# Optimization experiments

Measured on AMD Instinct MI355X. Metric: run time of the kernel, lower is better.

The kernel has to match this reference:

```python
import jax, jax.numpy as jnp
import numpy as np

B, T, N, D = 8, 24, 263, 512
N0, N1 = 32, 64
SEG = 12
LAMBDA_INIT = 0.8 - 0.6 * float(np.exp(-0.3 * (1 - 1)))  # layer_idx=1 -> 0.2


def _ln(x, g, b, eps=1e-5):
    m = jnp.mean(x, axis=-1, keepdims=True)
    v = jnp.var(x, axis=-1, keepdims=True)
    return (x - m) * jax.lax.rsqrt(v + eps) * g + b


def _proj(x, W):
    # 1x1 Conv2d over channel dim == per-position linear, W: [out, in]
    return jnp.einsum('btnd,ed->btne', x, W)


def _forward(x, agg_x0, agg_x1, tmp_map,
             Wq_s, Wk_s, Wv_s, lq1, lk1, lq2, lk2, ln_g, ln_b,
             Wq_a0, Wk_a0, Wv_a0, Wq_a1, Wk_a1, Wv_a1, M0, M1, Wagg, bagg,
             Wq_t, Wk_t, Wv_t, q_agg, Wk_tg, Wv_tg, Wout, bout):
    B, T, N, D = x.shape
    # ---- SpatialDiffAttn: spa_dim=256, heads=4, head_dim=32 (2*32 per head) ----
    H, dh = 4, 32
    q = _proj(x, Wq_s).reshape(B, T, N, H, 2 * dh)
    k = _proj(x, Wk_s).reshape(B, T, N, H, 2 * dh)
    v = _proj(x, Wv_s).reshape(B, T, N, H, 2 * dh)
    q1, q2 = q[..., :dh], q[..., dh:]
    k1, k2 = k[..., :dh], k[..., dh:]
    sc = dh ** -0.5
    # attn11/attn12 share softmax(q1 k1^T); cat([p1@v1, p1@v2]) == p1 @ v_full
    p1 = jax.nn.softmax(jnp.einsum('btnhd,btmhd->bthnm', q1, k1) * sc, axis=-1)
    a1 = jnp.einsum('bthnm,btmhe->btnhe', p1, v)
    p2 = jax.nn.softmax(jnp.einsum('btnhd,btmhd->bthnm', q2, k2) * sc, axis=-1)
    a2 = jnp.einsum('bthnm,btmhe->btnhe', p2, v)
    lam = jnp.exp(jnp.sum(lq1 * lk1)) - jnp.exp(jnp.sum(lq2 * lk2)) + LAMBDA_INIT
    s_x = (_ln(a1 - lam * a2, ln_g, ln_b) * (1.0 - LAMBDA_INIT)).reshape(B, T, N, H * 2 * dh)

    # ---- SpatialAttn aggregated branches (agg_dim=128, heads=2, head_dim=64) ----
    def agg_branch(ax, Wq, Wk, Wv, M):
        Ni = ax.shape[2]
        Ha, dha = 2, 64
        qa = _proj(ax, Wq).reshape(B, T, Ni, Ha, dha)
        ka = _proj(ax, Wk).reshape(B, T, Ni, Ha, dha)
        va = _proj(ax, Wv).reshape(B, T, Ni, Ha, dha)
        pa = jax.nn.softmax(jnp.einsum('btnhd,btmhd->bthnm', qa, ka) * (dha ** -0.5), axis=-1)
        sx = jnp.einsum('bthnm,btmhd->bthnd', pa, va)          # [B,T,Ha,Ni,dha]
        # cls_map = M^T -> pool Ni clusters up to N regions
        return jnp.einsum('mn,bthmd->btnhd', M, sx).reshape(B, T, N, Ha * dha)

    sg = agg_branch(agg_x0, Wq_a0, Wk_a0, Wv_a0, M0) + agg_branch(agg_x1, Wq_a1, Wk_a1, Wv_a1, M1)
    sg = sg @ Wagg.T + bagg

    # ---- TemporalAttn (tmp_dim=128, heads=2, head_dim=64) ----
    Ht, dht = 2, 64
    qt = _proj(x, Wq_t).reshape(B, T, N, Ht, dht)
    kt = _proj(x, Wk_t).reshape(B, T, N, Ht, dht)
    vt = _proj(x, Wv_t).reshape(B, T, N, Ht, dht)
    pt = jax.nn.softmax(jnp.einsum('btnhd,bsnhd->bnhts', qt, kt) * (dht ** -0.5), axis=-1)
    t_x = jnp.einsum('bnhts,bsnhd->btnhd', pt, vt).reshape(B, T, N, Ht * dht)

    # ---- TemporalAttn aggregated (learned query, seg_num=12) ----
    S = q_agg.shape[1]
    qg = q_agg.reshape(N, S, Ht, dht)
    kg = _proj(x, Wk_tg).reshape(B, T, N, Ht, dht)
    vg = _proj(x, Wv_tg).reshape(B, T, N, Ht, dht)
    pg = jax.nn.softmax(jnp.einsum('nshd,btnhd->bnhst', qg, kg) * (dht ** -0.5), axis=-1)
    tgx = jnp.einsum('bnhst,btnhd->bnshd', pg, vg).reshape(B, N, S, Ht * dht)
    tg = jnp.einsum('bnts,bnsd->btnd', tmp_map, tgx)           # [B,T,N,128]

    st = jnp.concatenate([s_x, sg, t_x, tg], axis=-1)          # [B,T,N,640]
    return st @ Wout.T + bout


def setup_inputs() -> dict:
    ks = jax.random.split(jax.random.key(0), 32)
    r = lambda i, shape, s=0.05: (jax.random.normal(ks[i], shape) * s).astype(jnp.float32)
    return dict(
        x=r(0, (B, T, N, D), 1.0),
        agg_x0=r(1, (B, T, N0, D), 1.0),
        agg_x1=r(2, (B, T, N1, D), 1.0),
        tmp_map=jax.random.uniform(ks[3], (B, N, T, SEG), dtype=jnp.float32),
        Wq_s=r(4, (256, D)), Wk_s=r(5, (256, D)), Wv_s=r(6, (256, D)),
        lq1=r(7, (32,), 0.1), lk1=r(8, (32,), 0.1), lq2=r(9, (32,), 0.1), lk2=r(10, (32,), 0.1),
        ln_g=jnp.ones((64,), jnp.float32), ln_b=jnp.zeros((64,), jnp.float32),
        Wq_a0=r(11, (128, D)), Wk_a0=r(12, (128, D)), Wv_a0=r(13, (128, D)),
        Wq_a1=r(14, (128, D)), Wk_a1=r(15, (128, D)), Wv_a1=r(16, (128, D)),
        M0=r(17, (N0, N), 0.1), M1=r(18, (N1, N), 0.1),
        Wagg=r(19, (128, 128)), bagg=jnp.zeros((128,), jnp.float32),
        Wq_t=r(20, (128, D)), Wk_t=r(21, (128, D)), Wv_t=r(22, (128, D)),
        q_agg=r(23, (N, SEG, 128), 1.0),
        Wk_tg=r(24, (128, D)), Wv_tg=r(25, (128, D)),
        Wout=r(26, (D, 640)), bout=jnp.zeros((D,), jnp.float32),
    )


def reference(x, agg_x0, agg_x1, tmp_map,
              Wq_s, Wk_s, Wv_s, lq1, lk1, lq2, lk2, ln_g, ln_b,
              Wq_a0, Wk_a0, Wv_a0, Wq_a1, Wk_a1, Wv_a1, M0, M1, Wagg, bagg,
              Wq_t, Wk_t, Wv_t, q_agg, Wk_tg, Wv_tg, Wout, bout):
    return _forward(x, agg_x0, agg_x1, tmp_map,
                    Wq_s, Wk_s, Wv_s, lq1, lk1, lq2, lk2, ln_g, ln_b,
                    Wq_a0, Wk_a0, Wv_a0, Wq_a1, Wk_a1, Wv_a1, M0, M1, Wagg, bagg,
                    Wq_t, Wk_t, Wv_t, q_agg, Wk_tg, Wv_tg, Wout, bout)
```

## Files before the change

### kernel.cpp

```cpp
#include <hip/hip_runtime.h>

#define NN 263
#define TT 24

typedef __fp16 h2 __attribute__((ext_vector_type(2)));
typedef _Float16 f16x4 __attribute__((ext_vector_type(4)));
typedef _Float16 f16x8 __attribute__((ext_vector_type(8)));
typedef float f32x4 __attribute__((ext_vector_type(4)));

struct WSegs  { const float* p[6]; };
struct WSegsH { const _Float16* p[6]; };
struct CvtSegs { const float* src[11]; _Float16* dst[11]; int cnt8[11]; };

static __device__ __forceinline__ float wred_sum(float v) {
  #pragma unroll
  for (int off = 32; off >= 1; off >>= 1) v += __shfl_xor(v, off, 64);
  return v;
}
static __device__ __forceinline__ float wred_max(float v) {
  #pragma unroll
  for (int off = 32; off >= 1; off >>= 1) v = fmaxf(v, __shfl_xor(v, off, 64));
  return v;
}

__global__ __launch_bounds__(256) void cvt_f16(CvtSegs cs, int nseg, int total8)
{
  const int stride = gridDim.x * 256;
  for (int i = blockIdx.x * 256 + threadIdx.x; i < total8; i += stride) {
    int r = i, s = 0;
    while (s < nseg - 1 && r >= cs.cnt8[s]) { r -= cs.cnt8[s]; ++s; }
    const float* sp = cs.src[s] + (size_t)r * 8;
    float4 a = *(const float4*)sp;
    float4 b = *(const float4*)(sp + 4);
    union { h2 h[4]; f16x8 v; } u;
    u.h[0] = __builtin_amdgcn_cvt_pkrtz(a.x, a.y);
    u.h[1] = __builtin_amdgcn_cvt_pkrtz(a.z, a.w);
    u.h[2] = __builtin_amdgcn_cvt_pkrtz(b.x, b.y);
    u.h[3] = __builtin_amdgcn_cvt_pkrtz(b.z, b.w);
    *(f16x8*)(cs.dst[s] + (size_t)r * 8) = u.v;
  }
}

template<int OUT_HALF>
__global__ __launch_bounds__(256) void gemm_h16(
    const _Float16* __restrict__ A, WSegsH wsg, const float* __restrict__ bias,
    void* __restrict__ Cp, int M, int NT, int K, int ldc)
{
  __shared__ _Float16 As[2][128][40];
  __shared__ _Float16 Bs[2][128][40];
  const int tid  = threadIdx.x;
  const int lane = tid & 63;
  const int wave = tid >> 6;
  const int wr = wave >> 1, wc = wave & 1;

  const int nwg = gridDim.x;
  const int q8 = nwg >> 3, r8 = nwg & 7;
  const int xcd = blockIdx.x & 7, pos = blockIdx.x >> 3;
  const int logical = (xcd < r8 ? xcd * (q8 + 1) : r8 * (q8 + 1) + (xcd - r8) * q8) + pos;
  const int bm = (logical / NT) * 128;
  const int bn = logical - (logical / NT) * NT;
  const _Float16* __restrict__ W = wsg.p[bn];

  const int srow = tid >> 2;
  const int sch  = (tid & 3) * 8;
  const _Float16* aptr[2];
  const _Float16* bptr[2];
  #pragma unroll
  for (int l = 0; l < 2; ++l) {
    int gm = bm + srow + 64 * l; if (gm > M - 1) gm = M - 1;
    aptr[l] = A + (size_t)gm * K + sch;
    bptr[l] = W + (size_t)(srow + 64 * l) * K + sch;
  }

  f32x4 acc[4][4];
  #pragma unroll
  for (int i = 0; i < 4; ++i)
    #pragma unroll
    for (int j = 0; j < 4; ++j) {
      acc[i][j].x = 0.f; acc[i][j].y = 0.f; acc[i][j].z = 0.f; acc[i][j].w = 0.f;
    }

  const int fr = lane & 15;
  const int fk = (lane >> 4) * 8;

  f16x8 av[2], bv[2];
  av[0] = *(const f16x8*)aptr[0]; av[1] = *(const f16x8*)aptr[1];
  bv[0] = *(const f16x8*)bptr[0]; bv[1] = *(const f16x8*)bptr[1];

  int cur = 0;
  for (int k0 = 0; k0 < K; k0 += 32, cur ^= 1) {
    *(f16x8*)&As[cur][srow     ][sch] = av[0];
    *(f16x8*)&As[cur][srow + 64][sch] = av[1];
    *(f16x8*)&Bs[cur][srow     ][sch] = bv[0];
    *(f16x8*)&Bs[cur][srow + 64][sch] = bv[1];
    if (k0 + 32 < K) {
      av[0] = *(const f16x8*)(aptr[0] + k0 + 32);
      av[1] = *(const f16x8*)(aptr[1] + k0 + 32);
      bv[0] = *(const f16x8*)(bptr[0] + k0 + 32);
      bv[1] = *(const f16x8*)(bptr[1] + k0 + 32);
    }
    __syncthreads();

    f16x8 af[4], bf[4];
    #pragma unroll
    for (int mi = 0; mi < 4; ++mi)
      af[mi] = *(const f16x8*)&As[cur][wr * 64 + mi * 16 + fr][fk];
    #pragma unroll
    for (int ni = 0; ni < 4; ++ni)
      bf[ni] = *(const f16x8*)&Bs[cur][wc * 64 + ni * 16 + fr][fk];
    #pragma unroll
    for (int mi = 0; mi < 4; ++mi)
      #pragma unroll
      for (int ni = 0; ni < 4; ++ni)
        acc[mi][ni] = __builtin_amdgcn_mfma_f32_16x16x32_f16(
            af[mi], bf[ni], acc[mi][ni], 0, 0, 0);
  }

  #pragma unroll
  for (int mi = 0; mi < 4; ++mi) {
    int rb = bm + wr * 64 + mi * 16 + (lane >> 4) * 4;
    #pragma unroll
    for (int r = 0; r < 4; ++r) {
      int gm = rb + r;
      if (gm < M) {
        int gn = bn * 128 + wc * 64 + fr;
        #pragma unroll
        for (int ni = 0; ni < 4; ++ni) {
          float v = acc[mi][ni][r];
          if (bias) v += bias[gn + ni * 16];
          if (OUT_HALF) {
            ((_Float16*)Cp)[(size_t)gm * ldc + gn + ni * 16] = (_Float16)v;
          } else {
            ((float*)Cp)[(size_t)gm * ldc + gn + ni * 16] = v;
          }
        }
      }
    }
  }
}

__global__ __launch_bounds__(256) void gemm_nt_mfma(
    const float* __restrict__ A, WSegs ws, const float* __restrict__ bias,
    float* __restrict__ C, int M, int NT, int K, int ldc)
{
  __shared__ _Float16 As[128][40];
  __shared__ _Float16 Bs[128][40];
  const int tid  = threadIdx.x;
  const int lane = tid & 63;
  const int wave = tid >> 6;
  const int wr = wave >> 1, wc = wave & 1;

  const int nwg = gridDim.x;
  const int q8 = nwg >> 3, r8 = nwg & 7;
  const int xcd = blockIdx.x & 7, pos = blockIdx.x >> 3;
  const int logical = (xcd < r8 ? xcd * (q8 + 1) : r8 * (q8 + 1) + (xcd - r8) * q8) + pos;
  const int bm = (logical / NT) * 128;
  const int bn = logical - (logical / NT) * NT;
  const float* __restrict__ W = ws.p[bn];

  const int srow = tid >> 3;
  const int skq  = (tid & 7) * 4;
  const float* aptr[4];
  const float* bptr[4];
  #pragma unroll
  for (int l = 0; l < 4; ++l) {
    int gm = bm + srow + 32 * l; if (gm > M - 1) gm = M - 1;
    aptr[l] = A + (size_t)gm * K + skq;
    bptr[l] = W + (size_t)(srow + 32 * l) * K + skq;
  }

  f32x4 acc[4][4];
  #pragma unroll
  for (int i = 0; i < 4; ++i)
    #pragma unroll
    for (int j = 0; j < 4; ++j) {
      acc[i][j].x = 0.f; acc[i][j].y = 0.f; acc[i][j].z = 0.f; acc[i][j].w = 0.f;
    }

  const int fr = lane & 15;
  const int fk = (lane >> 4) * 8;

  float4 av[4], bv[4];
  #pragma unroll
  for (int l = 0; l < 4; ++l) {
    av[l] = *(const float4*)(aptr[l]);
    bv[l] = *(const float4*)(bptr[l]);
  }

  for (int k0 = 0; k0 < K; k0 += 32) {
    #pragma unroll
    for (int l = 0; l < 4; ++l) {
      f16x4 a4, b4;
      a4.x = (_Float16)av[l].x; a4.y = (_Float16)av[l].y;
      a4.z = (_Float16)av[l].z; a4.w = (_Float16)av[l].w;
      b4.x = (_Float16)bv[l].x; b4.y = (_Float16)bv[l].y;
      b4.z = (_Float16)bv[l].z; b4.w = (_Float16)bv[l].w;
      *(f16x4*)&As[srow + 32 * l][skq] = a4;
      *(f16x4*)&Bs[srow + 32 * l][skq] = b4;
    }
    __syncthreads();

    if (k0 + 32 < K) {
      #pragma unroll
      for (int l = 0; l < 4; ++l) {
        av[l] = *(const float4*)(aptr[l] + k0 + 32);
        bv[l] = *(const float4*)(bptr[l] + k0 + 32);
      }
    }

    f16x8 af[4], bf[4];
    #pragma unroll
    for (int mi = 0; mi < 4; ++mi)
      af[mi] = *(const f16x8*)&As[wr * 64 + mi * 16 + fr][fk];
    #pragma unroll
    for (int ni = 0; ni < 4; ++ni)
      bf[ni] = *(const f16x8*)&Bs[wc * 64 + ni * 16 + fr][fk];
    #pragma unroll
    for (int mi = 0; mi < 4; ++mi)
      #pragma unroll
      for (int ni = 0; ni < 4; ++ni)
        acc[mi][ni] = __builtin_amdgcn_mfma_f32_16x16x32_f16(
            af[mi], bf[ni], acc[mi][ni], 0, 0, 0);
    __syncthreads();
  }

  #pragma unroll
  for (int mi = 0; mi < 4; ++mi) {
    int rb = bm + wr * 64 + mi * 16 + (lane >> 4) * 4;
    #pragma unroll
    for (int r = 0; r < 4; ++r) {
      int gm = rb + r;
      if (gm < M) {
        int gn = bn * 128 + wc * 64 + fr;
        float* crow = C + (size_t)gm * ldc + gn;
        #pragma unroll
        for (int ni = 0; ni < 4; ++ni) {
          float v = acc[mi][ni][r];
          if (bias) v += bias[gn + ni * 16];
          crow[ni * 16] = v;
        }
      }
    }
  }
}

__global__ void lam_kernel(const float* __restrict__ lq1, const float* __restrict__ lk1,
                           const float* __restrict__ lq2, const float* __restrict__ lk2,
                           float* __restrict__ out) {
  int lane = threadIdx.x;
  float v1 = lane < 32 ? lq1[lane] * lk1[lane] : 0.f;
  float v2 = lane < 32 ? lq2[lane] * lk2[lane] : 0.f;
  v1 = wred_sum(v1);
  v2 = wred_sum(v2);
  if (lane == 0) out[0] = expf(v1) - expf(v2) + 0.2f;
}

__global__ __launch_bounds__(512, 2) void diff_attn(
    const _Float16* __restrict__ qkv, _Float16* __restrict__ aout)
{
  __shared__ _Float16 Ks[2][272][40];
  __shared__ h2 Vt[64][148];
  __shared__ h2 Pb[8][16][148];

  const int h  = blockIdx.x & 3;
  const int bt = blockIdx.x >> 2;
  const int tid = threadIdx.x;
  const int lane = tid & 63;
  const int wave = tid >> 6;
  const int fr = lane & 15;
  const int kb = (lane >> 4) * 4;
  const _Float16* base = qkv + (size_t)bt * NN * 768;

  for (int idx = tid; idx < 272 * 8; idx += 512) {
    int row = idx >> 3, c = idx & 7;
    int sr = row < NN ? row : NN - 1;
    f16x8 kv = *(const f16x8*)(base + (size_t)sr * 768 + 256 + h * 64 + c * 8);
    *(f16x8*)&Ks[c >> 2][row][(c & 3) * 8] = kv;
  }
  {
    const ushort* vb = (const ushort*)(base + 512 + h * 64);
    for (int idx = tid; idx < 64 * 37; idx += 512) {
      int d = idx & 63, kp0 = (idx >> 6) * 4;
      union { ushort u[8]; f16x8 v; } w;
      #pragma unroll
      for (int i = 0; i < 4; ++i) {
        int kp = kp0 + i;
        ushort lo = 0, hi = 0;
        if (kp < 136) {
          int m0 = 2 * kp, m1 = 2 * kp + 1;
          if (m0 > NN - 1) m0 = NN - 1;
          if (m1 > NN - 1) m1 = NN - 1;
          lo = vb[(size_t)m0 * 768 + d];
          hi = vb[(size_t)m1 * 768 + d];
        }
        w.u[2 * i] = lo; w.u[2 * i + 1] = hi;
      }
      *(f16x8*)&Vt[d][kp0] = w.v;
    }
  }
  {
    h2 z; z.x = (__fp16)0.f; z.y = (__fp16)0.f;
    #pragma unroll
    for (int t = 0; t < 3; ++t) Pb[wave][fr][136 + (kb >> 2) * 3 + t] = z;
  }
  __syncthreads();

  const float scq = 0.17677669529663687f;

  for (int task = wave; task < 34; task += 8) {
    const int chunk = task >> 1;
    const int half  = task & 1;

    int qsrc = chunk * 16 + fr; if (qsrc > NN - 1) qsrc = NN - 1;
    f16x8 qf = *(const f16x8*)(base + (size_t)qsrc * 768 + h * 64 + half * 32 + kb * 2);

    f32x4 s[17];
    #pragma unroll
    for (int mt = 0; mt < 17; ++mt) {
      f16x8 af = *(const f16x8*)&Ks[half][mt * 16 + fr][kb * 2];
      f32x4 z4 = {0.f, 0.f, 0.f, 0.f};
      s[mt] = __builtin_amdgcn_mfma_f32_16x16x32_f16(af, qf, z4, 0, 0, 0);
    }

    float mx4[4] = {-1e30f, -1e30f, -1e30f, -1e30f};
    #pragma unroll
    for (int mt = 0; mt < 17; ++mt)
      #pragma unroll
      for (int r = 0; r < 4; ++r) {
        float v = s[mt][r] * scq;
        if (mt * 16 + kb + r >= NN) v = -1e30f;
        s[mt][r] = v;
        mx4[r] = fmaxf(mx4[r], v);
      }
    float mx = fmaxf(fmaxf(mx4[0], mx4[1]), fmaxf(mx4[2], mx4[3]));
    mx = fmaxf(mx, __shfl_xor(mx, 16, 64));
    mx = fmaxf(mx, __shfl_xor(mx, 32, 64));
    float sm4[4] = {0.f, 0.f, 0.f, 0.f};
    #pragma unroll
    for (int mt = 0; mt < 17; ++mt)
      #pragma unroll
      for (int r = 0; r < 4; ++r) {
        float p = __expf(s[mt][r] - mx);
        s[mt][r] = p;
        sm4[r] += p;
      }
    float sum = (sm4[0] + sm4[1]) + (sm4[2] + sm4[3]);
    sum += __shfl_xor(sum, 16, 64);
    sum += __shfl_xor(sum, 32, 64);
    float inv = 1.f / sum;

    #pragma unroll
    for (int mt = 0; mt < 17; ++mt) {
      union { h2 h[2]; f16x4 v; } pw;
      pw.h[0] = __builtin_amdgcn_cvt_pkrtz(s[mt][0] * inv, s[mt][1] * inv);
      pw.h[1] = __builtin_amdgcn_cvt_pkrtz(s[mt][2] * inv, s[mt][3] * inv);
      *(f16x4*)&Pb[wave][fr][8 * mt + (kb >> 1)] = pw.v;
    }

    f32x4 o[4];
    #pragma unroll
    for (int nt = 0; nt < 4; ++nt) {
      o[nt].x = 0.f; o[nt].y = 0.f; o[nt].z = 0.f; o[nt].w = 0.f;
    }
    #pragma unroll
    for (int s9 = 0; s9 < 9; ++s9) {
      f16x8 pa = *(const f16x8*)&Pb[wave][fr][16 * s9 + kb];
      #pragma unroll
      for (int nt = 0; nt < 4; ++nt) {
        f16x8 vb2 = *(const f16x8*)&Vt[nt * 16 + fr][16 * s9 + kb];
        o[nt] = __builtin_amdgcn_mfma_f32_16x16x32_f16(pa, vb2, o[nt], 0, 0, 0);
      }
    }

    _Float16* ab = aout + (size_t)half * (50496ull * 256ull);
    #pragma unroll
    for (int r = 0; r < 4; ++r) {
      int qrow = chunk * 16 + kb + r;
      if (qrow < NN) {
        _Float16* op = ab + ((size_t)(bt * NN + qrow) * 4 + h) * 64;
        #pragma unroll
        for (int nt = 0; nt < 4; ++nt) op[nt * 16 + fr] = (_Float16)o[nt][r];
      }
    }
  }
}

__global__ __launch_bounds__(256) void diff_ln(
    const _Float16* __restrict__ a1, const _Float16* __restrict__ a2,
    const float* __restrict__ lamp,
    const float* __restrict__ g, const float* __restrict__ b,
    _Float16* __restrict__ st)
{
  const int btn = blockIdx.x;
  const int lane = threadIdx.x & 63;
  const int h = threadIdx.x >> 6;
  const float lam = lamp[0];
  size_t off = ((size_t)btn * 4 + h) * 64 + lane;
  float y = (float)a1[off] - lam * (float)a2[off];
  float mean = wred_sum(y) * (1.f / 64.f);
  float t = y - mean;
  float var = wred_sum(t * t) * (1.f / 64.f);
  float r = rsqrtf(var + 1e-5f);
  st[(size_t)btn * 640 + h * 64 + lane] = (_Float16)((t * r * g[lane] + b[lane]) * 0.8f);
}

__global__ __launch_bounds__(256) void temporal_attn(
    const _Float16* __restrict__ qkvt, _Float16* __restrict__ st)
{
  __shared__ float qs[48][68];
  __shared__ float kt[48][68];
  __shared__ float vt[48][68];
  __shared__ float Ss[48][28];
  const int b = blockIdx.x / NN;
  const int n = blockIdx.x % NN;
  const int tid = threadIdx.x;
  const int lane = tid & 63;
  const int wave = tid >> 6;

  for (int idx = tid; idx < 48 * 16; idx += 256) {
    int row = idx >> 4, dq = (idx & 15) * 4;
    int h = row / 24, t = row - h * 24;
    const _Float16* g = qkvt + ((size_t)(b * TT + t) * NN + n) * 640 + h * 64 + dq;
    f16x4 a = *(const f16x4*)(g);
    f16x4 k = *(const f16x4*)(g + 128);
    f16x4 v = *(const f16x4*)(g + 256);
    float4 fa = {(float)a.x, (float)a.y, (float)a.z, (float)a.w};
    float4 fk = {(float)k.x, (float)k.y, (float)k.z, (float)k.w};
    float4 fv = {(float)v.x, (float)v.y, (float)v.z, (float)v.w};
    *(float4*)&qs[row][dq] = fa;
    *(float4*)&kt[row][dq] = fk;
    *(float4*)&vt[row][dq] = fv;
  }
  __syncthreads();

  for (int idx = tid; idx < 48 * 24; idx += 256) {
    int row = idx / 24, s = idx - row * 24;
    int krow = (row >= 24 ? 24 : 0) + s;
    float a0 = 0.f, a1 = 0.f, a2 = 0.f, a3 = 0.f;
    #pragma unroll
    for (int dq = 0; dq < 64; dq += 4) {
      float4 q = *(const float4*)&qs[row][dq];
      float4 k = *(const float4*)&kt[krow][dq];
      a0 = fmaf(q.x, k.x, a0);
      a1 = fmaf(q.y, k.y, a1);
      a2 = fmaf(q.z, k.z, a2);
      a3 = fmaf(q.w, k.w, a3);
    }
    Ss[row][s] = ((a0 + a1) + (a2 + a3)) * 0.125f;
  }
  __syncthreads();

  for (int r = wave; r < 48; r += 4) {
    float v = lane < 24 ? Ss[r][lane] : -1e30f;
    float mx = wred_max(v);
    float p = lane < 24 ? __expf(v - mx) : 0.f;
    float inv = 1.f / wred_sum(p);
    if (lane < 24) Ss[r][lane] = p * inv;
  }
  __syncthreads();

  for (int idx = tid; idx < 48 * 16; idx += 256) {
    int row = idx >> 4, dq = (idx & 15) * 4;
    int h = row / 24, t = row - h * 24;
    int bs = h * 24;
    float ax = 0.f, ay = 0.f, az = 0.f, aw = 0.f;
    #pragma unroll
    for (int s = 0; s < 24; ++s) {
      float p = Ss[row][s];
      float4 v = *(const float4*)&vt[bs + s][dq];
      ax = fmaf(p, v.x, ax);
      ay = fmaf(p, v.y, ay);
      az = fmaf(p, v.z, az);
      aw = fmaf(p, v.w, aw);
    }
    union { h2 h[2]; f16x4 v; } o2;
    o2.h[0] = __builtin_amdgcn_cvt_pkrtz(ax, ay);
    o2.h[1] = __builtin_amdgcn_cvt_pkrtz(az, aw);
    *(f16x4*)(st + ((size_t)(b * TT + t) * NN + n) * 640 + 384 + h * 64 + dq) = o2.v;
  }
}

__global__ __launch_bounds__(256) void tglobal_attn(
    const _Float16* __restrict__ qkvt, const float* __restrict__ q_agg,
    const float* __restrict__ tmp_map, _Float16* __restrict__ st)
{
  __shared__ float qg[24][68];
  __shared__ float kg[48][68];
  __shared__ float vg[48][68];
  __shared__ float Sg[24][28];
  __shared__ float tgx[12][128];
  const int b = blockIdx.x / NN;
  const int n = blockIdx.x % NN;
  const int tid = threadIdx.x;
  const int lane = tid & 63;
  const int wave = tid >> 6;

  for (int idx = tid; idx < 48 * 16; idx += 256) {
    int row = idx >> 4, dq = (idx & 15) * 4;
    int h = row / 24, t = row - h * 24;
    const _Float16* g = qkvt + ((size_t)(b * TT + t) * NN + n) * 640 + 384 + h * 64 + dq;
    f16x4 k = *(const f16x4*)(g);
    f16x4 v = *(const f16x4*)(g + 128);
    float4 fk = {(float)k.x, (float)k.y, (float)k.z, (float)k.w};
    float4 fv = {(float)v.x, (float)v.y, (float)v.z, (float)v.w};
    *(float4*)&kg[row][dq] = fk;
    *(float4*)&vg[row][dq] = fv;
  }
  for (int idx = tid; idx < 24 * 16; idx += 256) {
    int row = idx >> 4, dq = (idx & 15) * 4;
    int h = row / 12, s = row - h * 12;
    *(float4*)&qg[row][dq] =
        *(const float4*)(q_agg + ((size_t)n * 12 + s) * 128 + h * 64 + dq);
  }
  __syncthreads();

  for (int idx = tid; idx < 24 * 24; idx += 256) {
    int row = idx / 24, t = idx - row * 24;
    int krow = (row >= 12 ? 24 : 0) + t;
    float a0 = 0.f, a1 = 0.f, a2 = 0.f, a3 = 0.f;
    #pragma unroll
    for (int dq = 0; dq < 64; dq += 4) {
      float4 q = *(const float4*)&qg[row][dq];
      float4 k = *(const float4*)&kg[krow][dq];
      a0 = fmaf(q.x, k.x, a0);
      a1 = fmaf(q.y, k.y, a1);
      a2 = fmaf(q.z, k.z, a2);
      a3 = fmaf(q.w, k.w, a3);
    }
    Sg[row][t] = ((a0 + a1) + (a2 + a3)) * 0.125f;
  }
  __syncthreads();

  for (int r = wave; r < 24; r += 4) {
    float v = lane < 24 ? Sg[r][lane] : -1e30f;
    float mx = wred_max(v);
    float p = lane < 24 ? __expf(v - mx) : 0.f;
    float inv = 1.f / wred_sum(p);
    if (lane < 24) Sg[r][lane] = p * inv;
  }
  __syncthreads();

  for (int idx = tid; idx < 24 * 16; idx += 256) {
    int row = idx >> 4, dq = (idx & 15) * 4;
    int h = row / 12, s = row - h * 12;
    int bt_ = h * 24;
    float ax = 0.f, ay = 0.f, az = 0.f, aw = 0.f;
    #pragma unroll
    for (int t = 0; t < 24; ++t) {
      float p = Sg[row][t];
      float4 v = *(const float4*)&vg[bt_ + t][dq];
      ax = fmaf(p, v.x, ax);
      ay = fmaf(p, v.y, ay);
      az = fmaf(p, v.z, az);
      aw = fmaf(p, v.w, aw);
    }
    float4 o = {ax, ay, az, aw};
    *(float4*)&tgx[s][h * 64 + dq] = o;
  }
  __syncthreads();

  for (int idx = tid; idx < 24 * 32; idx += 256) {
    int t = idx >> 5, cq = (idx & 31) * 4;
    const float* tm = tmp_map + ((size_t)(b * NN + n) * TT + t) * 12;
    float ax = 0.f, ay = 0.f, az = 0.f, aw = 0.f;
    #pragma unroll
    for (int s = 0; s < 12; ++s) {
      float m = tm[s];
      float4 v = *(const float4*)&tgx[s][cq];
      ax = fmaf(m, v.x, ax);
      ay = fmaf(m, v.y, ay);
      az = fmaf(m, v.z, az);
      aw = fmaf(m, v.w, aw);
    }
    union { h2 h[2]; f16x4 v; } o2;
    o2.h[0] = __builtin_amdgcn_cvt_pkrtz(ax, ay);
    o2.h[1] = __builtin_amdgcn_cvt_pkrtz(az, aw);
    *(f16x4*)(st + ((size_t)(b * TT + t) * NN + n) * 640 + 512 + cq) = o2.v;
  }
}

__global__ __launch_bounds__(256) void agg_attn(
    const float* __restrict__ qkva, float* __restrict__ sx, int Ni, int lg)
{
  __shared__ float qa[64][68];
  __shared__ float ka[64][68];
  __shared__ float va[64][68];
  __shared__ float Ss[64][68];
  const int h = blockIdx.x & 1;
  const int bt = blockIdx.x >> 1;
  const int tid = threadIdx.x;
  const int lane = tid & 63;
  const int wave = tid >> 6;

  for (int idx = tid; idx < Ni * 16; idx += 256) {
    int m = idx >> 4, dq = (idx & 15) * 4;
    const float* r = qkva + (size_t)(bt * Ni + m) * 384 + h * 64 + dq;
    *(float4*)&qa[m][dq] = *(const float4*)(r);
    *(float4*)&ka[m][dq] = *(const float4*)(r + 128);
    *(float4*)&va[m][dq] = *(const float4*)(r + 256);
  }
  __syncthreads();

  for (int idx = tid; idx < Ni * Ni; idx += 256) {
    int n = idx >> lg, m = idx & (Ni - 1);
    float a0 = 0.f, a1 = 0.f, a2 = 0.f, a3 = 0.f;
    #pragma unroll
    for (int dq = 0; dq < 64; dq += 4) {
      float4 q = *(const float4*)&qa[n][dq];
      float4 k = *(const float4*)&ka[m][dq];
      a0 = fmaf(q.x, k.x, a0);
      a1 = fmaf(q.y, k.y, a1);
      a2 = fmaf(q.z, k.z, a2);
      a3 = fmaf(q.w, k.w, a3);
    }
    Ss[n][m] = ((a0 + a1) + (a2 + a3)) * 0.125f;
  }
  __syncthreads();

  for (int r = wave; r < Ni; r += 4) {
    float v = lane < Ni ? Ss[r][lane] : -1e30f;
    float mx = wred_max(v);
    float p = lane < Ni ? __expf(v - mx) : 0.f;
    float inv = 1.f / wred_sum(p);
    if (lane < Ni) Ss[r][lane] = p * inv;
  }
  __syncthreads();

  for (int idx = tid; idx < Ni * 16; idx += 256) {
    int n = idx >> 4, dq = (idx & 15) * 4;
    float ax = 0.f, ay = 0.f, az = 0.f, aw = 0.f;
    for (int m = 0; m < Ni; ++m) {
      float p = Ss[n][m];
      float4 v = *(const float4*)&va[m][dq];
      ax = fmaf(p, v.x, ax);
      ay = fmaf(p, v.y, ay);
      az = fmaf(p, v.z, az);
      aw = fmaf(p, v.w, aw);
    }
    float4 o = {ax, ay, az, aw};
    *(float4*)(sx + (size_t)(bt * Ni + n) * 128 + h * 64 + dq) = o;
  }
}

__global__ __launch_bounds__(256) void mmap_kernel(
    const float* __restrict__ sx0, const float* __restrict__ sx1,
    const float* __restrict__ M0, const float* __restrict__ M1,
    _Float16* __restrict__ sg)
{
  __shared__ float sS[96][128];
  __shared__ float Mc[96][88];
  const int bt = blockIdx.x;
  const int chunk = blockIdx.y;
  const int tid = threadIdx.x;
  const int nbase = chunk * 88;

  for (int idx = tid; idx < 96 * 32; idx += 256) {
    int m = idx >> 5, c4 = (idx & 31) * 4;
    float4 v = (m < 32)
        ? *(const float4*)(sx0 + ((size_t)(bt * 32 + m) * 128 + c4))
        : *(const float4*)(sx1 + ((size_t)(bt * 64 + (m - 32)) * 128 + c4));
    *(float4*)&sS[m][c4] = v;
  }
  for (int idx = tid; idx < 96 * 88; idx += 256) {
    int m = idx / 88, nl = idx - m * 88;
    int n = nbase + nl; if (n > NN - 1) n = NN - 1;
    Mc[m][nl] = (m < 32) ? M0[m * NN + n] : M1[(m - 32) * NN + n];
  }
  __syncthreads();

  for (int idx = tid; idx < 352; idx += 256) {
    const int n0 = (idx >> 5) * 8;
    const int c4 = (idx & 31) * 4;
    f32x4 acc[8];
    #pragma unroll
    for (int j = 0; j < 8; ++j) {
      acc[j].x = 0.f; acc[j].y = 0.f; acc[j].z = 0.f; acc[j].w = 0.f;
    }
    #pragma unroll 4
    for (int m = 0; m < 96; ++m) {
      float4 sv = *(const float4*)&sS[m][c4];
      float mj[8];
      *(float4*)&mj[0] = *(const float4*)&Mc[m][n0];
      *(float4*)&mj[4] = *(const float4*)&Mc[m][n0 + 4];
      #pragma unroll
      for (int j = 0; j < 8; ++j) {
        acc[j].x = fmaf(mj[j], sv.x, acc[j].x);
        acc[j].y = fmaf(mj[j], sv.y, acc[j].y);
        acc[j].z = fmaf(mj[j], sv.z, acc[j].z);
        acc[j].w = fmaf(mj[j], sv.w, acc[j].w);
      }
    }
    #pragma unroll
    for (int j = 0; j < 8; ++j) {
      int n = nbase + n0 + j;
      if (n < NN) {
        union { h2 h[2]; f16x4 v; } o;
        o.h[0] = __builtin_amdgcn_cvt_pkrtz(acc[j].x, acc[j].y);
        o.h[1] = __builtin_amdgcn_cvt_pkrtz(acc[j].z, acc[j].w);
        *(f16x4*)(sg + ((size_t)bt * NN + n) * 128 + c4) = o.v;
      }
    }
  }
}

extern "C" void kernel_launch(void* const* d_in, const int* in_sizes, int n_in,
                              void* d_out, int out_size, void* d_ws, size_t ws_size,
                              hipStream_t stream)
{
  const float* x       = (const float*)d_in[0];
  const float* agg_x0  = (const float*)d_in[1];
  const float* agg_x1  = (const float*)d_in[2];
  const float* tmp_map = (const float*)d_in[3];
  const float* Wq_s = (const float*)d_in[4];
  const float* Wk_s = (const float*)d_in[5];
  const float* Wv_s = (const float*)d_in[6];
  const float* lq1 = (const float*)d_in[7];
  const float* lk1 = (const float*)d_in[8];
  const float* lq2 = (const float*)d_in[9];
  const float* lk2 = (const float*)d_in[10];
  const float* ln_g = (const float*)d_in[11];
  const float* ln_b = (const float*)d_in[12];
  const float* Wq_a0 = (const float*)d_in[13];
  const float* Wk_a0 = (const float*)d_in[14];
  const float* Wv_a0 = (const float*)d_in[15];
  const float* Wq_a1 = (const float*)d_in[16];
  const float* Wk_a1 = (const float*)d_in[17];
  const float* Wv_a1 = (const float*)d_in[18];
  const float* M0   = (const float*)d_in[19];
  const float* M1   = (const float*)d_in[20];
  const float* Wagg = (const float*)d_in[21];
  const float* bagg = (const float*)d_in[22];
  const float* Wq_t = (const float*)d_in[23];
  const float* Wk_t = (const float*)d_in[24];
  const float* Wv_t = (const float*)d_in[25];
  const float* q_agg = (const float*)d_in[26];
  const float* Wk_tg = (const float*)d_in[27];
  const float* Wv_tg = (const float*)d_in[28];
  const float* Wout  = (const float*)d_in[29];
  const float* bout  = (const float*)d_in[30];
  float* ws  = (float*)d_ws;
  float* out = (float*)d_out;

  const size_t o_lam  = 1114112;
  const size_t o_A    = 1114128;
  const size_t o_qkvt = o_A + 38780928;
  const size_t o_B    = o_qkvt + 32317440;

  float* lamp  = ws + o_lam;
  _Float16* qkv_h  = (_Float16*)(ws + o_A);
  _Float16* st_h   = (_Float16*)(ws + o_A);
  _Float16* qkvt_h = (_Float16*)(ws + o_qkvt);
  _Float16* x_h = (_Float16*)(ws + o_B);
  _Float16* a1_h = (_Float16*)(ws + o_B);
  float* qkva0 = ws + o_B;
  float* qkva1 = qkva0 + 2359296;
  float* sx0   = qkva0 + 7077888;
  float* sx1   = qkva0 + 7864320;
  _Float16* sg_h = (_Float16*)(qkva0 + 9437184);
  _Float16* Wh  = (_Float16*)ws;

  hipLaunchKernelGGL(lam_kernel, dim3(1), dim3(64), 0, stream, lq1, lk1, lq2, lk2, lamp);

  CvtSegs cs;
  cs.src[0] = x;      cs.dst[0] = x_h;          cs.cnt8[0] = 25853952 / 8;
  cs.src[1] = Wq_s;   cs.dst[1] = Wh + 0;       cs.cnt8[1] = 131072 / 8;
  cs.src[2] = Wk_s;   cs.dst[2] = Wh + 131072;  cs.cnt8[2] = 131072 / 8;
  cs.src[3] = Wv_s;   cs.dst[3] = Wh + 262144;  cs.cnt8[3] = 131072 / 8;
  cs.src[4] = Wq_t;   cs.dst[4] = Wh + 393216;  cs.cnt8[4] = 65536 / 8;
  cs.src[5] = Wk_t;   cs.dst[5] = Wh + 458752;  cs.cnt8[5] = 65536 / 8;
  cs.src[6] = Wv_t;   cs.dst[6] = Wh + 524288;  cs.cnt8[6] = 65536 / 8;
  cs.src[7] = Wk_tg;  cs.dst[7] = Wh + 589824;  cs.cnt8[7] = 65536 / 8;
  cs.src[8] = Wv_tg;  cs.dst[8] = Wh + 655360;  cs.cnt8[8] = 65536 / 8;
  cs.src[9] = Wagg;   cs.dst[9] = Wh + 720896;  cs.cnt8[9] = 16384 / 8;
  cs.src[10] = Wout;  cs.dst[10] = Wh + 737280; cs.cnt8[10] = 327680 / 8;
  hipLaunchKernelGGL(cvt_f16, dim3(2048), dim3(256), 0, stream, cs, 11, 3364864);

  const int Mx = 50496;

  WSegsH wqkv; wqkv.p[0] = Wh; wqkv.p[1] = Wh + 65536;
  wqkv.p[2] = Wh + 131072; wqkv.p[3] = Wh + 196608;
  wqkv.p[4] = Wh + 262144; wqkv.p[5] = Wh + 327680;
  hipLaunchKernelGGL((gemm_h16<1>), dim3(395 * 6), dim3(256), 0, stream,
                     x_h, wqkv, (const float*)nullptr, (void*)qkv_h, Mx, 6, 512, 768);

  WSegsH wt; wt.p[0] = Wh + 393216; wt.p[1] = Wh + 458752; wt.p[2] = Wh + 524288;
  wt.p[3] = Wh + 589824; wt.p[4] = Wh + 655360; wt.p[5] = Wh + 393216;
  hipLaunchKernelGGL((gemm_h16<1>), dim3(395 * 5), dim3(256), 0, stream,
                     x_h, wt, (const float*)nullptr, (void*)qkvt_h, Mx, 5, 512, 640);

  hipLaunchKernelGGL(diff_attn, dim3(768), dim3(512), 0, stream, qkv_h, a1_h);
  hipLaunchKernelGGL(diff_ln, dim3(Mx), dim3(256), 0, stream,
                     a1_h, a1_h + 12926976, lamp, ln_g, ln_b, st_h);
  hipLaunchKernelGGL(temporal_attn, dim3(8 * NN), dim3(256), 0, stream, qkvt_h, st_h);
  hipLaunchKernelGGL(tglobal_attn, dim3(8 * NN), dim3(256), 0, stream, qkvt_h, q_agg, tmp_map, st_h);

  WSegs wa0; wa0.p[0] = Wq_a0; wa0.p[1] = Wk_a0; wa0.p[2] = Wv_a0;
  wa0.p[3] = wa0.p[4] = wa0.p[5] = Wq_a0;
  hipLaunchKernelGGL(gemm_nt_mfma, dim3(48 * 3), dim3(256), 0, stream,
                     agg_x0, wa0, (const float*)nullptr, qkva0, 6144, 3, 512, 384);
  WSegs wa1; wa1.p[0] = Wq_a1; wa1.p[1] = Wk_a1; wa1.p[2] = Wv_a1;
  wa1.p[3] = wa1.p[4] = wa1.p[5] = Wq_a1;
  hipLaunchKernelGGL(gemm_nt_mfma, dim3(96 * 3), dim3(256), 0, stream,
                     agg_x1, wa1, (const float*)nullptr, qkva1, 12288, 3, 512, 384);

  hipLaunchKernelGGL(agg_attn, dim3(384), dim3(256), 0, stream, qkva0, sx0, 32, 5);
  hipLaunchKernelGGL(agg_attn, dim3(384), dim3(256), 0, stream, qkva1, sx1, 64, 6);
  hipLaunchKernelGGL(mmap_kernel, dim3(192, 3), dim3(256), 0, stream, sx0, sx1, M0, M1, sg_h);

  WSegsH wag; wag.p[0] = Wh + 720896;
  wag.p[1] = wag.p[2] = wag.p[3] = wag.p[4] = wag.p[5] = wag.p[0];
  hipLaunchKernelGGL((gemm_h16<1>), dim3(395 * 1), dim3(256), 0, stream,
                     sg_h, wag, bagg, (void*)(st_h + 256), Mx, 1, 128, 640);

  WSegsH wo; wo.p[0] = Wh + 737280; wo.p[1] = Wh + 737280 + 81920;
  wo.p[2] = Wh + 737280 + 163840; wo.p[3] = Wh + 737280 + 245760;
  wo.p[4] = wo.p[5] = wo.p[0];
  hipLaunchKernelGGL((gemm_h16<0>), dim3(395 * 4), dim3(256), 0, stream,
                     st_h, wo, bout, (void*)out, Mx, 4, 640, 512);
}
```

Measured before the change: 839.3 us.

## Store spatial QKV and attention outputs head-major for contiguous per-head access

The QKV GEMM gets a new output mode that writes each 64-column slice into its own head-major plane, laid out as [plane][row][64] instead of row-interleaved with a stride of 768. diff_attn now reads K, V and Q from these contiguous per-head planes and writes its outputs in the same plane layout, and diff_ln indexes to match. The aim is fewer scattered strided loads when staging each head's K and V tiles, especially the 2-byte V transpose gathers. The GEMM epilogue still writes 64-wide row segments, so its store efficiency should be about the same.

```diff
diff --git a/kernel.cpp b/kernel.cpp
--- a/kernel.cpp
+++ b/kernel.cpp
@@ -41,7 +41,7 @@
   }
 }
 
-template<int OUT_HALF>
+template<int OUT_MODE>
 __global__ __launch_bounds__(256) void gemm_h16(
     const _Float16* __restrict__ A, WSegsH wsg, const float* __restrict__ bias,
     void* __restrict__ Cp, int M, int NT, int K, int ldc)
@@ -123,14 +123,26 @@
     for (int r = 0; r < 4; ++r) {
       int gm = rb + r;
       if (gm < M) {
-        int gn = bn * 128 + wc * 64 + fr;
-        #pragma unroll
-        for (int ni = 0; ni < 4; ++ni) {
-          float v = acc[mi][ni][r];
-          if (bias) v += bias[gn + ni * 16];
-          if (OUT_HALF) {
+        if (OUT_MODE == 2) {
+          _Float16* sb = (_Float16*)Cp
+              + (size_t)(bn * 2 + wc) * (50496ull * 64ull) + (size_t)gm * 64;
+          #pragma unroll
+          for (int ni = 0; ni < 4; ++ni)
+            sb[ni * 16 + fr] = (_Float16)acc[mi][ni][r];
+        } else if (OUT_MODE == 1) {
+          int gn = bn * 128 + wc * 64 + fr;
+          #pragma unroll
+          for (int ni = 0; ni < 4; ++ni) {
+            float v = acc[mi][ni][r];
+            if (bias) v += bias[gn + ni * 16];
             ((_Float16*)Cp)[(size_t)gm * ldc + gn + ni * 16] = (_Float16)v;
-          } else {
+          }
+        } else {
+          int gn = bn * 128 + wc * 64 + fr;
+          #pragma unroll
+          for (int ni = 0; ni < 4; ++ni) {
+            float v = acc[mi][ni][r];
+            if (bias) v += bias[gn + ni * 16];
             ((float*)Cp)[(size_t)gm * ldc + gn + ni * 16] = v;
           }
         }
@@ -269,16 +281,19 @@
   const int wave = tid >> 6;
   const int fr = lane & 15;
   const int kb = (lane >> 4) * 4;
-  const _Float16* base = qkv + (size_t)bt * NN * 768;
+  const size_t S = 50496ull * 64ull;
+  const _Float16* qh = qkv + (size_t)h * S       + (size_t)bt * NN * 64;
+  const _Float16* kh = qkv + (size_t)(4 + h) * S + (size_t)bt * NN * 64;
+  const _Float16* vh = qkv + (size_t)(8 + h) * S + (size_t)bt * NN * 64;
 
   for (int idx = tid; idx < 272 * 8; idx += 512) {
     int row = idx >> 3, c = idx & 7;
     int sr = row < NN ? row : NN - 1;
-    f16x8 kv = *(const f16x8*)(base + (size_t)sr * 768 + 256 + h * 64 + c * 8);
+    f16x8 kv = *(const f16x8*)(kh + (size_t)sr * 64 + c * 8);
     *(f16x8*)&Ks[c >> 2][row][(c & 3) * 8] = kv;
   }
   {
-    const ushort* vb = (const ushort*)(base + 512 + h * 64);
+    const ushort* vb = (const ushort*)vh;
     for (int idx = tid; idx < 64 * 37; idx += 512) {
       int d = idx & 63, kp0 = (idx >> 6) * 4;
       union { ushort u[8]; f16x8 v; } w;
@@ -290,8 +305,8 @@
           int m0 = 2 * kp, m1 = 2 * kp + 1;
           if (m0 > NN - 1) m0 = NN - 1;
           if (m1 > NN - 1) m1 = NN - 1;
-          lo = vb[(size_t)m0 * 768 + d];
-          hi = vb[(size_t)m1 * 768 + d];
+          lo = vb[(size_t)m0 * 64 + d];
+          hi = vb[(size_t)m1 * 64 + d];
         }
         w.u[2 * i] = lo; w.u[2 * i + 1] = hi;
       }
@@ -312,7 +327,7 @@
     const int half  = task & 1;
 
     int qsrc = chunk * 16 + fr; if (qsrc > NN - 1) qsrc = NN - 1;
-    f16x8 qf = *(const f16x8*)(base + (size_t)qsrc * 768 + h * 64 + half * 32 + kb * 2);
+    f16x8 qf = *(const f16x8*)(qh + (size_t)qsrc * 64 + half * 32 + kb * 2);
 
     f32x4 s[17];
     #pragma unroll
@@ -372,12 +387,12 @@
       }
     }
 
-    _Float16* ab = aout + (size_t)half * (50496ull * 256ull);
+    _Float16* ab = aout + (size_t)(half * 4 + h) * S + (size_t)bt * NN * 64;
     #pragma unroll
     for (int r = 0; r < 4; ++r) {
       int qrow = chunk * 16 + kb + r;
       if (qrow < NN) {
-        _Float16* op = ab + ((size_t)(bt * NN + qrow) * 4 + h) * 64;
+        _Float16* op = ab + (size_t)qrow * 64;
         #pragma unroll
         for (int nt = 0; nt < 4; ++nt) op[nt * 16 + fr] = (_Float16)o[nt][r];
       }
@@ -395,7 +410,7 @@
   const int lane = threadIdx.x & 63;
   const int h = threadIdx.x >> 6;
   const float lam = lamp[0];
-  size_t off = ((size_t)btn * 4 + h) * 64 + lane;
+  size_t off = ((size_t)h * 50496 + btn) * 64 + lane;
   float y = (float)a1[off] - lam * (float)a2[off];
   float mean = wred_sum(y) * (1.f / 64.f);
   float t = y - mean;
@@ -780,7 +795,7 @@
   WSegsH wqkv; wqkv.p[0] = Wh; wqkv.p[1] = Wh + 65536;
   wqkv.p[2] = Wh + 131072; wqkv.p[3] = Wh + 196608;
   wqkv.p[4] = Wh + 262144; wqkv.p[5] = Wh + 327680;
-  hipLaunchKernelGGL((gemm_h16<1>), dim3(395 * 6), dim3(256), 0, stream,
+  hipLaunchKernelGGL((gemm_h16<2>), dim3(395 * 6), dim3(256), 0, stream,
                      x_h, wqkv, (const float*)nullptr, (void*)qkv_h, Mx, 6, 512, 768);
 
   WSegsH wt; wt.p[0] = Wh + 393216; wt.p[1] = Wh + 458752; wt.p[2] = Wh + 524288;
```

Measured after the change: 842.6 us. No clear change (+0.4%).
